# Kernel optimization log

Hardware: AMD Instinct MI355X
Metric: run time of the kernel (lower is better)

The kernel has to match this reference:

```python
import jax, jax.numpy as jnp
import numpy as np

N = 200000   # nodes
R = 4        # relations
E = 1000000  # edges per relation
B = 1024     # graphs in batch


def _graph_conv(h, s, d, ew, W, b):
    """DGL GraphConv, norm='both', optional edge_weight. h:[N,F_in] -> [N,F_out]."""
    n = h.shape[0]
    ones = jnp.ones(s.shape[0], dtype=h.dtype)
    out_deg = jnp.clip(jax.ops.segment_sum(ones, s, num_segments=n), 1.0)
    in_deg = jnp.clip(jax.ops.segment_sum(ones, d, num_segments=n), 1.0)
    hs = h * jax.lax.rsqrt(out_deg)[:, None]          # src-side norm
    m = hs[s]                                         # gather: [E, F_in]
    if ew is not None:
        m = m * ew[:, None]
    agg = jax.ops.segment_sum(m, d, num_segments=n)   # scatter-sum: [N, F_in]
    rst = agg * jax.lax.rsqrt(in_deg)[:, None]        # dst-side norm
    return rst @ W + b


def _hetero_layer(h, src, dst, ew, W, b):
    out = None
    for r in range(R):
        ewr = None if ew is None else ew[r]
        o = _graph_conv(h, src[r], dst[r], ewr, W[r], b[r])
        out = o if out is None else out + o
    return out


def setup_inputs() -> dict:
    key = jax.random.key(0)
    ks = jax.random.split(key, 10)
    feat = jax.random.normal(ks[0], (N, 2), dtype=jnp.float32)
    src = jax.random.randint(ks[1], (R, E), 0, N, dtype=jnp.int32)
    dst = jax.random.randint(ks[2], (R, E), 0, N, dtype=jnp.int32)
    ew = jax.random.uniform(ks[3], (R, E), dtype=jnp.float32)
    graph_ids = jnp.sort(jax.random.randint(ks[4], (N,), 0, B, dtype=jnp.int32))
    W1 = jax.random.normal(ks[5], (R, 2, 16), dtype=jnp.float32) * 0.5
    b1 = jnp.zeros((R, 16), dtype=jnp.float32)
    W2 = jax.random.normal(ks[6], (R, 16, 16), dtype=jnp.float32) * 0.25
    b2 = jnp.zeros((R, 16), dtype=jnp.float32)
    Wc = jax.random.normal(ks[7], (16, 2), dtype=jnp.float32) * 0.25
    bc = jnp.zeros((2,), dtype=jnp.float32)
    return {"feat": feat, "src": src, "dst": dst, "ew": ew,
            "graph_ids": graph_ids, "W1": W1, "b1": b1,
            "W2": W2, "b2": b2, "Wc": Wc, "bc": bc}


def reference(feat, src, dst, ew, graph_ids, W1, b1, W2, b2, Wc, bc):
    # layer 1: per-relation weighted GraphConv, summed over relations
    h = _hetero_layer(feat, src, dst, ew, W1, b1)
    h = jax.nn.relu(h)
    # layer 2: no edge weights (kwargs not forwarded in original code)
    h = _hetero_layer(h, src, dst, None, W2, b2)
    # mean_nodes per graph in the batch
    sums = jax.ops.segment_sum(h, graph_ids, num_segments=B)          # [B,16]
    cnts = jax.ops.segment_sum(jnp.ones((N,), h.dtype), graph_ids, num_segments=B)
    hg = sums / jnp.clip(cnts, 1.0)[:, None]
    return hg @ Wc + bc                                               # [B,2]
```

## Files before the change

kernel.cpp:

```cpp
#include <hip/hip_runtime.h>
#include <hip/hip_fp16.h>

#define NN 200000
#define RR 4
#define EE 1000000
#define BB 1024
#define RN (RR*NN)

#define BSH 7
#define BSZ 128
#define NB 1563
#define RK (RR*NB)
#define CSH 10
#define CNODES 1024
#define CC 196
#define EPB 8192
#define SBT 1024
#define BPR ((EE + EPB - 1) / EPB)
#define GSLOTS 32

#define SRC_OF(u)  (((u) >> 7) & 0x3FFFF)
#define DL_OF(u)   ((int)((u) & 127))
#define DEG_OF(u)  ((u) >> 25)

#define OFF_POOL    0
#define OFF_CNT     (OFF_POOL + BB*16)
#define OFF_CNTS    (OFF_CNT + BB)
#define OFF_CNTD    (OFF_CNTS + RR*CC)
#define OFF_CURS    (OFF_CNTD + RR*CC)
#define OFF_CURD    (OFF_CURS + RR*CC)
#define OFF_GSB     (OFF_CURD + RR*CC)
#define OFF_GDB     (OFF_GSB + RR*CC + 1)
#define OFF_GFIN    (OFF_GDB + RR*CC + 1)
#define ZERO_UNITS_ (OFF_GFIN + RK + 1)
#define ZERO_UNITS  (ZERO_UNITS_ + (ZERO_UNITS_ & 1))
#define OFF_DEGB    ZERO_UNITS
#define OFF_INVI    (OFF_DEGB + RN/4)
#define OFF_RW16    (OFF_INVI + RN)
#define OFF_AGG1    (OFF_RW16 + RN/2)
#define OFF_SBC     OFF_AGG1
#define OFF_H1H     (OFF_AGG1 + RN*2)
#define OFF_KWC_    (OFF_H1H + NN*8)
#define OFF_KWC     (OFF_KWC_ + (OFF_KWC_ & 1))
#define OFF_KW4     (OFF_KWC + RR*EE*2)


__global__ __launch_bounds__(1024) void k_cnt(const int* __restrict__ src,
                                              const int* __restrict__ dst,
                                              int* __restrict__ cntS,
                                              int* __restrict__ cntD) {
  __shared__ int hS[CC], hD[CC];
  int t = threadIdx.x, r = blockIdx.y, c0 = blockIdx.x * EPB;
  if (t < CC) { hS[t] = 0; hD[t] = 0; }
  __syncthreads();
  for (int i = t; i < EPB; i += 1024) {
    int e = c0 + i;
    if (e < EE) {
      atomicAdd(&hS[src[r * EE + e] >> CSH], 1);
      atomicAdd(&hD[dst[r * EE + e] >> CSH], 1);
    }
  }
  __syncthreads();
  if (t < CC) {
    if (hS[t]) atomicAdd(&cntS[r * CC + t], hS[t]);
    if (hD[t]) atomicAdd(&cntD[r * CC + t], hD[t]);
  }
}

__global__ __launch_bounds__(1024) void k_scan(const int* __restrict__ cntS,
                                               const int* __restrict__ cntD,
                                               int* __restrict__ gsb,
                                               int* __restrict__ gdb,
                                               int* __restrict__ gfin) {
  __shared__ int s[1024];
  int t = threadIdx.x;
  int v = (t < RR * CC) ? cntS[t] : 0;
  s[t] = v;
  __syncthreads();
  for (int off = 1; off < 1024; off <<= 1) {
    int u = (t >= off) ? s[t - off] : 0;
    __syncthreads();
    s[t] += u;
    __syncthreads();
  }
  if (t < RR * CC) {
    int r = t / CC;
    int pre = (r == 0) ? 0 : s[r * CC - 1];
    gsb[t] = r * EE + (s[t] - v) - pre;
  }
  if (t == 0) gsb[RR * CC] = RR * EE;
  __syncthreads();
  int w = (t < RR * CC) ? cntD[t] : 0;
  s[t] = w;
  __syncthreads();
  for (int off = 1; off < 1024; off <<= 1) {
    int u = (t >= off) ? s[t - off] : 0;
    __syncthreads();
    s[t] += u;
    __syncthreads();
  }
  if (t < RR * CC) {
    int r = t / CC;
    int pre = (r == 0) ? 0 : s[r * CC - 1];
    gdb[t] = r * EE + (s[t] - w) - pre;
  }
  if (t == 0) { gdb[RR * CC] = RR * EE; gfin[RK] = RR * EE; }
}

__global__ __launch_bounds__(SBT) void k_part(const int* __restrict__ src,
                                              const int* __restrict__ dst,
                                              const float* __restrict__ ew,
                                              const int* __restrict__ gsb,
                                              const int* __restrict__ gdb,
                                              int* __restrict__ curS,
                                              int* __restrict__ curD,
                                              unsigned short* __restrict__ sbc,
                                              unsigned long long* __restrict__ kwc) {
  __shared__ int cS[CC], bS[CC], lS[CC];
  __shared__ int cD[CC], bD[CC], lD[CC];
  int t = threadIdx.x, r = blockIdx.y, c0 = blockIdx.x * EPB;
  if (t < CC) { cS[t] = 0; cD[t] = 0; }
  __syncthreads();
  for (int i = t; i < EPB; i += SBT) {
    int e = c0 + i;
    if (e < EE) {
      atomicAdd(&cS[src[r * EE + e] >> CSH], 1);
      atomicAdd(&cD[dst[r * EE + e] >> CSH], 1);
    }
  }
  __syncthreads();
  if (t < CC) {
    int kc = r * CC + t;
    int v = cS[t]; bS[t] = v ? gsb[kc] + atomicAdd(&curS[kc], v) : 0; lS[t] = 0;
    int w = cD[t]; bD[t] = w ? gdb[kc] + atomicAdd(&curD[kc], w) : 0; lD[t] = 0;
  }
  __syncthreads();
  for (int i = t; i < EPB; i += SBT) {
    int e = c0 + i;
    if (e < EE) {
      int idx = r * EE + e;
      int s = src[idx], d = dst[idx];
      int cs = s >> CSH;
      sbc[(size_t)bS[cs] + atomicAdd(&lS[cs], 1)] = (unsigned short)(s & (CNODES - 1));
      int cd = d >> CSH;
      unsigned low = (unsigned)(d & (CNODES - 1)) | ((unsigned)s << CSH);
      unsigned long long rec =
          ((unsigned long long)__half_as_ushort(__float2half_rn(ew[idx])) << 32) | low;
      kwc[(size_t)bD[cd] + atomicAdd(&lD[cd], 1)] = rec;
    }
  }
}

__global__ __launch_bounds__(1024) void k_fineS(const unsigned short* __restrict__ sbc,
                                                const int* __restrict__ gsb,
                                                unsigned char* __restrict__ degb) {
  __shared__ int h[CNODES];
  int t = threadIdx.x, c = blockIdx.x, r = blockIdx.y;
  int kc = r * CC + c;
  int s0 = gsb[kc];
  int m = gsb[kc + 1] - s0;
  h[t] = 0;
  __syncthreads();
  for (int i = t; i < m; i += 1024) atomicAdd(&h[sbc[(size_t)s0 + i]], 1);
  __syncthreads();
  int n = c * CNODES + t;
  if (n < NN) degb[r * NN + n] = (unsigned char)min(max(h[t], 1), 63);
}

__global__ __launch_bounds__(1024) void k_fineD(const unsigned long long* __restrict__ kwc,
                                                const int* __restrict__ gdb,
                                                const unsigned char* __restrict__ degb,
                                                const float* __restrict__ feat,
                                                unsigned* __restrict__ kw4,
                                                int* __restrict__ gfin,
                                                float* __restrict__ invi,
                                                unsigned short* __restrict__ rw16,
                                                float* __restrict__ agg1) {
  __shared__ int h[CNODES];
  __shared__ float la[CNODES * 2];
  __shared__ int s4[1024];
  __shared__ int sfb[8];
  int t = threadIdx.x, c = blockIdx.x, r = blockIdx.y;
  int kc = r * CC + c;
  int b0 = gdb[kc];
  int nrec = gdb[kc + 1] - b0;
  h[t] = 0; la[t] = 0.f; la[t + CNODES] = 0.f;
  __syncthreads();
  for (int i = t; i < nrec; i += 1024)
    atomicAdd(&h[(unsigned)kwc[(size_t)b0 + i] & (CNODES - 1)], 1);
  __syncthreads();
  int cntt = h[t];
  s4[t] = cntt;
  __syncthreads();
  for (int off = 1; off < 1024; off <<= 1) {
    int v = (t >= off) ? s4[t - off] : 0;
    __syncthreads();
    s4[t] += v;
    __syncthreads();
  }
  int base = s4[t] - cntt;
  if ((t & 127) == 0) sfb[t >> 7] = base;
  __syncthreads();
  int n0 = c * CNODES;
  {
    int n = n0 + t;
    if (n < NN) {
      invi[r * NN + n] = rsqrtf((float)max(cntt, 1));
      rw16[r * NN + n] = (unsigned short)(base - sfb[t >> 7]);
    }
  }
  if (t < 8) {
    int kb = c * 8 + t;
    if (kb < NB) gfin[r * NB + kb] = b0 + sfb[t];
  }
  __syncthreads();
  h[t] = base;
  __syncthreads();
  for (int i = t; i < nrec; i += 1024) {
    unsigned long long rc = kwc[(size_t)b0 + i];
    unsigned low = (unsigned)rc;
    int dcl = low & (CNODES - 1);
    int s = low >> CSH;
    float ewf = __half2float(__ushort_as_half((unsigned short)(rc >> 32)));
    unsigned dg = degb[r * NN + s];
    float w1 = ewf * rsqrtf((float)dg);
    float2 fv = ((const float2*)feat)[s];
    atomicAdd(&la[dcl * 2],     fv.x * w1);
    atomicAdd(&la[dcl * 2 + 1], fv.y * w1);
    int pos = atomicAdd(&h[dcl], 1);
    kw4[(size_t)b0 + pos] = ((unsigned)dcl & 127u) | ((unsigned)s << 7) | (dg << 25);
  }
  __syncthreads();
  {
    int n = n0 + t;
    if (n < NN)
      ((float2*)agg1)[r * NN + n] = make_float2(la[t * 2], la[t * 2 + 1]);
  }
}

__device__ __forceinline__ unsigned pack2h(float a, float b) {
  __half2 h = __floats2half2_rn(a, b);
  return *reinterpret_cast<unsigned*>(&h);
}

__global__ __launch_bounds__(256) void k_l1b(const float* __restrict__ agg1,
                                             const float* __restrict__ invi,
                                             const float* __restrict__ W1,
                                             const float* __restrict__ b1,
                                             __half* __restrict__ h1h) {
  __shared__ float sW[RR * 2 * 16];
  __shared__ float sb[16];
  int t = threadIdx.x, b = blockIdx.x;
  if (t < RR * 2 * 16) sW[t] = W1[t];
  if (t < 16) {
    float s = 0.f;
    for (int r = 0; r < RR; r++) s += b1[r * 16 + t];
    sb[t] = s;
  }
  __syncthreads();
  int n = b * 256 + t;
  if (n >= NN) return;
  float acc[16];
#pragma unroll
  for (int j = 0; j < 16; j++) acc[j] = sb[j];
#pragma unroll
  for (int r = 0; r < RR; r++) {
    float iv = invi[r * NN + n];
    float2 a = ((const float2*)agg1)[r * NN + n];
    float a0 = a.x * iv, a1 = a.y * iv;
#pragma unroll
    for (int j = 0; j < 16; j++)
      acc[j] += a0 * sW[(r * 2 + 0) * 16 + j] + a1 * sW[(r * 2 + 1) * 16 + j];
  }
#pragma unroll
  for (int j = 0; j < 16; j++) acc[j] = fmaxf(acc[j], 0.f);
  uint4 u0, u1;
  u0.x = pack2h(acc[0], acc[1]);  u0.y = pack2h(acc[2], acc[3]);
  u0.z = pack2h(acc[4], acc[5]);  u0.w = pack2h(acc[6], acc[7]);
  u1.x = pack2h(acc[8], acc[9]);  u1.y = pack2h(acc[10], acc[11]);
  u1.z = pack2h(acc[12], acc[13]); u1.w = pack2h(acc[14], acc[15]);
  uint4* o = (uint4*)(h1h + (size_t)n * 16);
  o[0] = u0; o[1] = u1;
}

__device__ __forceinline__ void acc8(float* acc, uint4 u, float w) {
  float2 p;
  p = __half22float2(*(__half2*)&u.x); acc[0] += p.x * w; acc[1] += p.y * w;
  p = __half22float2(*(__half2*)&u.y); acc[2] += p.x * w; acc[3] += p.y * w;
  p = __half22float2(*(__half2*)&u.z); acc[4] += p.x * w; acc[5] += p.y * w;
  p = __half22float2(*(__half2*)&u.w); acc[6] += p.x * w; acc[7] += p.y * w;
}

__global__ __launch_bounds__(256) void k_l2(const unsigned* __restrict__ kw4,
                                            const int* __restrict__ gfin,
                                            const unsigned short* __restrict__ rw16,
                                            const __half* __restrict__ h1h,
                                            const float* __restrict__ invi,
                                            const float* __restrict__ W2,
                                            const int* __restrict__ gid,
                                            float* __restrict__ pool,
                                            float* __restrict__ cnt) {
  __shared__ float agg[BSZ * 17];
  __shared__ float sW4[RR * 256];
  __shared__ int   sg[BSZ];
  __shared__ unsigned short srw[BSZ + 2];
  __shared__ float gslot[GSLOTS * 16];
  __shared__ int   cslot[GSLOTS];
  __shared__ int   present[GSLOTS];
  int t = threadIdx.x, b = blockIdx.x;
  int n0 = b << BSH;
#pragma unroll
  for (int r = 0; r < RR; r++) sW4[r * 256 + t] = W2[r * 256 + t];
  if (t < GSLOTS) { cslot[t] = 0; present[t] = 0; }
  for (int i = t; i < GSLOTS * 16; i += 256) gslot[i] = 0.f;
  int n = n0 + t;
  bool valid = (t < BSZ) && (n < NN);
  float out[16];
#pragma unroll
  for (int j = 0; j < 16; j++) out[j] = 0.f;
  const uint4* h4p = (const uint4*)h1h;
  int f8 = t & 1, g = t >> 1;

  for (int r = 0; r < RR; r++) {
    int k = r * NB + b;
    int base = gfin[k];
    int m = gfin[k + 1] - base;
    __syncthreads();
    if (t < BSZ) {
      int nn_ = n0 + t;
      srw[t] = (nn_ < NN) ? rw16[r * NN + nn_] : (unsigned short)m;
    }
    if (t == BSZ) srw[BSZ] = (unsigned short)m;
    __syncthreads();
    const unsigned* rb = kw4 + (size_t)base;
    int e = srw[g], en = srw[g + 1];
    float acc[8];
#pragma unroll
    for (int j = 0; j < 8; j++) acc[j] = 0.f;
    for (; e + 3 < en; e += 4) {
      unsigned r0 = rb[e], r1 = rb[e + 1], r2 = rb[e + 2], r3 = rb[e + 3];
      uint4 u0 = h4p[(size_t)SRC_OF(r0) * 2 + f8];
      uint4 u1 = h4p[(size_t)SRC_OF(r1) * 2 + f8];
      uint4 u2 = h4p[(size_t)SRC_OF(r2) * 2 + f8];
      uint4 u3 = h4p[(size_t)SRC_OF(r3) * 2 + f8];
      acc8(acc, u0, rsqrtf((float)DEG_OF(r0)));
      acc8(acc, u1, rsqrtf((float)DEG_OF(r1)));
      acc8(acc, u2, rsqrtf((float)DEG_OF(r2)));
      acc8(acc, u3, rsqrtf((float)DEG_OF(r3)));
    }
    for (; e < en; e++) {
      unsigned rr = rb[e];
      uint4 u = h4p[(size_t)SRC_OF(rr) * 2 + f8];
      acc8(acc, u, rsqrtf((float)DEG_OF(rr)));
    }
#pragma unroll
    for (int j = 0; j < 8; j++) agg[g * 17 + 8 * f8 + j] = acc[j];
    __syncthreads();
    if (valid) {
      float iv = invi[r * NN + n];
#pragma unroll
      for (int kk = 0; kk < 16; kk++) {
        float a = agg[t * 17 + kk] * iv;
#pragma unroll
        for (int j = 0; j < 16; j++) out[j] += a * sW4[r * 256 + kk * 16 + j];
      }
    }
  }
  __syncthreads();
  int g0 = gid[n0];
  if (t < BSZ) {
    sg[t] = valid ? (gid[n] - g0) : -1;
#pragma unroll
    for (int j = 0; j < 16; j++) agg[t * 17 + j] = out[j];
  }
  __syncthreads();
  {
    int f = t & 15, i0 = t >> 4;
    for (int i = i0; i < BSZ; i += 16) {
      int gsN = sg[i];
      if (gsN < 0) continue;
      float v = agg[i * 17 + f];
      if (gsN < GSLOTS) {
        atomicAdd(&gslot[gsN * 16 + f], v);
        if (f == 0) {
          present[gsN] = 1;
          atomicAdd(&cslot[gsN], 1);
        }
      } else {
        atomicAdd(&pool[(g0 + gsN) * 16 + f], v);
        if (f == 0) atomicAdd(&cnt[g0 + gsN], 1.0f);
      }
    }
  }
  __syncthreads();
  if (t < GSLOTS * 16) {
    int gsN = t >> 4, f = t & 15;
    if (present[gsN]) atomicAdd(&pool[(g0 + gsN) * 16 + f], gslot[t]);
  }
  if (t < GSLOTS && cslot[t] > 0)
    atomicAdd(&cnt[g0 + t], (float)cslot[t]);
}

__global__ __launch_bounds__(256) void k_final(const float* __restrict__ pool,
                                               const float* __restrict__ cnt,
                                               const float* __restrict__ b2,
                                               const float* __restrict__ Wc,
                                               const float* __restrict__ bc,
                                               float* __restrict__ out) {
  int b = blockIdx.x * 256 + threadIdx.x;
  if (b >= BB) return;
  float c = cnt[b];
  float inv = 1.0f / fmaxf(c, 1.0f);
  float o0 = bc[0], o1 = bc[1];
#pragma unroll
  for (int j = 0; j < 16; j++) {
    float sb = 0.f;
    for (int r = 0; r < RR; r++) sb += b2[r * 16 + j];
    float v = (pool[b * 16 + j] + c * sb) * inv;
    o0 += v * Wc[j * 2 + 0];
    o1 += v * Wc[j * 2 + 1];
  }
  out[b * 2 + 0] = o0;
  out[b * 2 + 1] = o1;
}

extern "C" void kernel_launch(void* const* d_in, const int* in_sizes, int n_in,
                              void* d_out, int out_size, void* d_ws, size_t ws_size,
                              hipStream_t stream) {
  const float* feat = (const float*)d_in[0];
  const int*   src  = (const int*)d_in[1];
  const int*   dst  = (const int*)d_in[2];
  const float* ew   = (const float*)d_in[3];
  const int*   gid  = (const int*)d_in[4];
  const float* W1   = (const float*)d_in[5];
  const float* b1   = (const float*)d_in[6];
  const float* W2   = (const float*)d_in[7];
  const float* b2   = (const float*)d_in[8];
  const float* Wc   = (const float*)d_in[9];
  const float* bc   = (const float*)d_in[10];

  char* ws = (char*)d_ws;
  float* pool   = (float*)(ws + (size_t)OFF_POOL * 4);
  float* cnt    = (float*)(ws + (size_t)OFF_CNT  * 4);
  int*   cntS   = (int*)  (ws + (size_t)OFF_CNTS * 4);
  int*   cntD   = (int*)  (ws + (size_t)OFF_CNTD * 4);
  int*   curS   = (int*)  (ws + (size_t)OFF_CURS * 4);
  int*   curD   = (int*)  (ws + (size_t)OFF_CURD * 4);
  int*   gsb    = (int*)  (ws + (size_t)OFF_GSB  * 4);
  int*   gdb    = (int*)  (ws + (size_t)OFF_GDB  * 4);
  int*   gfin   = (int*)  (ws + (size_t)OFF_GFIN * 4);
  unsigned char*  degb = (unsigned char*) (ws + (size_t)OFF_DEGB * 4);
  float* invi   = (float*)(ws + (size_t)OFF_INVI * 4);
  unsigned short* rw16 = (unsigned short*)(ws + (size_t)OFF_RW16 * 4);
  float* agg1   = (float*)(ws + (size_t)OFF_AGG1 * 4);
  unsigned short* sbc  = (unsigned short*)(ws + (size_t)OFF_SBC * 4);
  __half* h1h   = (__half*)(ws + (size_t)OFF_H1H * 4);
  unsigned long long* kwc = (unsigned long long*)(ws + (size_t)OFF_KWC * 4);
  unsigned* kw4 = (unsigned*)(ws + (size_t)OFF_KW4 * 4);

  hipMemsetAsync(d_ws, 0, (size_t)ZERO_UNITS * 4, stream);

  k_cnt   <<<dim3(BPR, RR), 1024, 0, stream>>>(src, dst, cntS, cntD);
  k_scan  <<<1, 1024, 0, stream>>>(cntS, cntD, gsb, gdb, gfin);
  k_part  <<<dim3(BPR, RR), SBT, 0, stream>>>(src, dst, ew, gsb, gdb, curS, curD, sbc, kwc);
  k_fineS <<<dim3(CC, RR), 1024, 0, stream>>>(sbc, gsb, degb);
  k_fineD <<<dim3(CC, RR), 1024, 0, stream>>>(kwc, gdb, degb, feat, kw4, gfin, invi, rw16, agg1);
  k_l1b   <<<(NN + 255) / 256, 256, 0, stream>>>(agg1, invi, W1, b1, h1h);
  k_l2    <<<NB, 256, 0, stream>>>(kw4, gfin, rw16, h1h, invi, W2, gid, pool, cnt);
  k_final <<<(BB + 255) / 256, 256, 0, stream>>>(pool, cnt, b2, Wc, bc, (float*)d_out);
}
```

Before: 319.2 us.

## Vectorize edge partition loads and interleave relations in layer-2 gather

```diff
diff --git a/kernel.cpp b/kernel.cpp
--- a/kernel.cpp
+++ b/kernel.cpp
@@ -14,7 +14,7 @@
 #define CSH 10
 #define CNODES 1024
 #define CC 196
-#define EPB 8192
+#define EPB 16384
 #define SBT 1024
 #define BPR ((EE + EPB - 1) / EPB)
 #define GSLOTS 32
@@ -53,12 +53,15 @@
   int t = threadIdx.x, r = blockIdx.y, c0 = blockIdx.x * EPB;
   if (t < CC) { hS[t] = 0; hD[t] = 0; }
   __syncthreads();
-  for (int i = t; i < EPB; i += 1024) {
-    int e = c0 + i;
-    if (e < EE) {
-      atomicAdd(&hS[src[r * EE + e] >> CSH], 1);
-      atomicAdd(&hD[dst[r * EE + e] >> CSH], 1);
-    }
+  const int4* s4p = (const int4*)(src + (size_t)r * EE + c0);
+  const int4* d4p = (const int4*)(dst + (size_t)r * EE + c0);
+  int nv = min(EPB, EE - c0) >> 2;
+  for (int i = t; i < nv; i += 1024) {
+    int4 s = s4p[i], d = d4p[i];
+    atomicAdd(&hS[s.x >> CSH], 1); atomicAdd(&hS[s.y >> CSH], 1);
+    atomicAdd(&hS[s.z >> CSH], 1); atomicAdd(&hS[s.w >> CSH], 1);
+    atomicAdd(&hD[d.x >> CSH], 1); atomicAdd(&hD[d.y >> CSH], 1);
+    atomicAdd(&hD[d.z >> CSH], 1); atomicAdd(&hD[d.w >> CSH], 1);
   }
   __syncthreads();
   if (t < CC) {
@@ -121,12 +124,16 @@
   int t = threadIdx.x, r = blockIdx.y, c0 = blockIdx.x * EPB;
   if (t < CC) { cS[t] = 0; cD[t] = 0; }
   __syncthreads();
-  for (int i = t; i < EPB; i += SBT) {
-    int e = c0 + i;
-    if (e < EE) {
-      atomicAdd(&cS[src[r * EE + e] >> CSH], 1);
-      atomicAdd(&cD[dst[r * EE + e] >> CSH], 1);
-    }
+  const int4*   s4p = (const int4*)  (src + (size_t)r * EE + c0);
+  const int4*   d4p = (const int4*)  (dst + (size_t)r * EE + c0);
+  const float4* e4p = (const float4*)(ew  + (size_t)r * EE + c0);
+  int nv = min(EPB, EE - c0) >> 2;
+  for (int i = t; i < nv; i += SBT) {
+    int4 s = s4p[i], d = d4p[i];
+    atomicAdd(&cS[s.x >> CSH], 1); atomicAdd(&cS[s.y >> CSH], 1);
+    atomicAdd(&cS[s.z >> CSH], 1); atomicAdd(&cS[s.w >> CSH], 1);
+    atomicAdd(&cD[d.x >> CSH], 1); atomicAdd(&cD[d.y >> CSH], 1);
+    atomicAdd(&cD[d.z >> CSH], 1); atomicAdd(&cD[d.w >> CSH], 1);
   }
   __syncthreads();
   if (t < CC) {
@@ -135,17 +142,21 @@
     int w = cD[t]; bD[t] = w ? gdb[kc] + atomicAdd(&curD[kc], w) : 0; lD[t] = 0;
   }
   __syncthreads();
-  for (int i = t; i < EPB; i += SBT) {
-    int e = c0 + i;
-    if (e < EE) {
-      int idx = r * EE + e;
-      int s = src[idx], d = dst[idx];
+  for (int i = t; i < nv; i += SBT) {
+    int4 s4 = s4p[i], d4 = d4p[i];
+    float4 w4 = e4p[i];
+    int ss[4] = {s4.x, s4.y, s4.z, s4.w};
+    int dd[4] = {d4.x, d4.y, d4.z, d4.w};
+    float we[4] = {w4.x, w4.y, w4.z, w4.w};
+#pragma unroll
+    for (int j = 0; j < 4; j++) {
+      int s = ss[j], d = dd[j];
       int cs = s >> CSH;
       sbc[(size_t)bS[cs] + atomicAdd(&lS[cs], 1)] = (unsigned short)(s & (CNODES - 1));
       int cd = d >> CSH;
       unsigned low = (unsigned)(d & (CNODES - 1)) | ((unsigned)s << CSH);
       unsigned long long rec =
-          ((unsigned long long)__half_as_ushort(__float2half_rn(ew[idx])) << 32) | low;
+          ((unsigned long long)__half_as_ushort(__float2half_rn(we[j])) << 32) | low;
       kwc[(size_t)bD[cd] + atomicAdd(&lD[cd], 1)] = rec;
     }
   }
@@ -161,7 +172,16 @@
   int m = gsb[kc + 1] - s0;
   h[t] = 0;
   __syncthreads();
-  for (int i = t; i < m; i += 1024) atomicAdd(&h[sbc[(size_t)s0 + i]], 1);
+  int head = (s0 & 1) && (m > 0) ? 1 : 0;
+  if (head && t == 0) atomicAdd(&h[sbc[s0]], 1);
+  int mv = (m - head) >> 1;
+  const unsigned* p = (const unsigned*)(sbc + s0 + head);
+  for (int i = t; i < mv; i += 1024) {
+    unsigned v = p[i];
+    atomicAdd(&h[v & 0xFFFF], 1);
+    atomicAdd(&h[v >> 16], 1);
+  }
+  if (((m - head) & 1) && t == 1023) atomicAdd(&h[sbc[(size_t)s0 + m - 1]], 1);
   __syncthreads();
   int n = c * CNODES + t;
   if (n < NN) degb[r * NN + n] = (unsigned char)min(max(h[t], 1), 63);
@@ -303,7 +323,7 @@
   __shared__ float agg[BSZ * 17];
   __shared__ float sW4[RR * 256];
   __shared__ int   sg[BSZ];
-  __shared__ unsigned short srw[BSZ + 2];
+  __shared__ unsigned short srw4[RR][BSZ + 1];
   __shared__ float gslot[GSLOTS * 16];
   __shared__ int   cslot[GSLOTS];
   __shared__ int   present[GSLOTS];
@@ -315,46 +335,56 @@
   for (int i = t; i < GSLOTS * 16; i += 256) gslot[i] = 0.f;
   int n = n0 + t;
   bool valid = (t < BSZ) && (n < NN);
-  float out[16];
-#pragma unroll
-  for (int j = 0; j < 16; j++) out[j] = 0.f;
+  int base[RR], mr[RR];
+#pragma unroll
+  for (int r = 0; r < RR; r++) {
+    base[r] = gfin[r * NB + b];
+    mr[r] = gfin[r * NB + b + 1] - base[r];
+  }
+#pragma unroll
+  for (int r = 0; r < RR; r++) {
+    if (t < BSZ) srw4[r][t] = (n < NN) ? rw16[r * NN + n] : (unsigned short)mr[r];
+    if (t == BSZ) srw4[r][BSZ] = (unsigned short)mr[r];
+  }
+  __syncthreads();
   const uint4* h4p = (const uint4*)h1h;
   int f8 = t & 1, g = t >> 1;
-
+  int e[RR], en[RR];
+  float acc[RR][8];
+#pragma unroll
   for (int r = 0; r < RR; r++) {
-    int k = r * NB + b;
-    int base = gfin[k];
-    int m = gfin[k + 1] - base;
-    __syncthreads();
-    if (t < BSZ) {
-      int nn_ = n0 + t;
-      srw[t] = (nn_ < NN) ? rw16[r * NN + nn_] : (unsigned short)m;
+    e[r] = srw4[r][g];
+    en[r] = srw4[r][g + 1];
+#pragma unroll
+    for (int j = 0; j < 8; j++) acc[r][j] = 0.f;
+  }
+  for (;;) {
+    bool any = false;
+    uint4 u[RR]; float w[RR]; bool act[RR];
+#pragma unroll
+    for (int r = 0; r < RR; r++) {
+      act[r] = e[r] < en[r];
+      if (act[r]) {
+        unsigned rr = kw4[(size_t)base[r] + e[r]];
+        u[r] = h4p[(size_t)SRC_OF(rr) * 2 + f8];
+        w[r] = rsqrtf((float)DEG_OF(rr));
+        e[r]++;
+        any = true;
+      }
     }
-    if (t == BSZ) srw[BSZ] = (unsigned short)m;
-    __syncthreads();
-    const unsigned* rb = kw4 + (size_t)base;
-    int e = srw[g], en = srw[g + 1];
-    float acc[8];
-#pragma unroll
-    for (int j = 0; j < 8; j++) acc[j] = 0.f;
-    for (; e + 3 < en; e += 4) {
-      unsigned r0 = rb[e], r1 = rb[e + 1], r2 = rb[e + 2], r3 = rb[e + 3];
-      uint4 u0 = h4p[(size_t)SRC_OF(r0) * 2 + f8];
-      uint4 u1 = h4p[(size_t)SRC_OF(r1) * 2 + f8];
-      uint4 u2 = h4p[(size_t)SRC_OF(r2) * 2 + f8];
-      uint4 u3 = h4p[(size_t)SRC_OF(r3) * 2 + f8];
-      acc8(acc, u0, rsqrtf((float)DEG_OF(r0)));
-      acc8(acc, u1, rsqrtf((float)DEG_OF(r1)));
-      acc8(acc, u2, rsqrtf((float)DEG_OF(r2)));
-      acc8(acc, u3, rsqrtf((float)DEG_OF(r3)));
-    }
-    for (; e < en; e++) {
-      unsigned rr = rb[e];
-      uint4 u = h4p[(size_t)SRC_OF(rr) * 2 + f8];
-      acc8(acc, u, rsqrtf((float)DEG_OF(rr)));
-    }
-#pragma unroll
-    for (int j = 0; j < 8; j++) agg[g * 17 + 8 * f8 + j] = acc[j];
+    if (!any) break;
+#pragma unroll
+    for (int r = 0; r < RR; r++)
+      if (act[r]) acc8(acc[r], u[r], w[r]);
+  }
+  float out[16];
+#pragma unroll
+  for (int j = 0; j < 16; j++) out[j] = 0.f;
+#pragma unroll
+  for (int r = 0; r < RR; r++) {
+    __syncthreads();
+#pragma unroll
+    for (int j = 0; j < 8; j++) agg[g * 17 + 8 * f8 + j] = acc[r][j];
     __syncthreads();
     if (valid) {
       float iv = invi[r * NN + n];
```

New measurement: 473.8 us. 48.4% more time.
